# Optimization experiments

Measured on AMD Instinct MI355X. Metric: run time of the kernel, lower is better.

Reference implementation:

```python
import jax, jax.numpy as jnp
import numpy as np

N = 100000      # nodes
E = 1600000     # edges (avg degree 16)
IN = 128        # in_channels
OUT = 32        # out_channels -> hidden = 2*OUT = 64


def gcn_conv(x, src, dst, W, b):
    """PyG GCNConv: linear transform, add self loops, symmetric D^-1/2 (A+I) D^-1/2 aggregation."""
    n = x.shape[0]
    h = x @ W                                   # [N, out]
    # degree with self loops (all edge weights = 1)
    deg = jax.ops.segment_sum(jnp.ones(src.shape[0], h.dtype), dst, num_segments=n) + 1.0
    dinv = jax.lax.rsqrt(deg)                   # [N]
    norm = dinv[src] * dinv[dst]                # [E]
    agg = jax.ops.segment_sum(h[src] * norm[:, None], dst, num_segments=n)
    agg = agg + h * (dinv * dinv)[:, None]      # self-loop contribution
    return agg + b


def setup_inputs() -> dict:
    key = jax.random.key(0)
    ks = jax.random.split(key, 8)
    x = jax.random.normal(ks[0], (N, IN), jnp.float32)
    edge_index = jax.random.randint(ks[1], (2, E), 0, N, jnp.int32)
    H = 2 * OUT
    W1 = jax.random.normal(ks[2], (IN, H), jnp.float32) / jnp.sqrt(jnp.float32(IN))
    b1 = jnp.zeros((H,), jnp.float32)
    W_mu = jax.random.normal(ks[3], (H, OUT), jnp.float32) / jnp.sqrt(jnp.float32(H))
    b_mu = jnp.zeros((OUT,), jnp.float32)
    W_logstd = jax.random.normal(ks[4], (H, OUT), jnp.float32) / jnp.sqrt(jnp.float32(H))
    b_logstd = jnp.zeros((OUT,), jnp.float32)
    return {"x": x, "edge_index": edge_index, "W1": W1, "b1": b1,
            "W_mu": W_mu, "b_mu": b_mu, "W_logstd": W_logstd, "b_logstd": b_logstd}


def reference(x, edge_index, W1, b1, W_mu, b_mu, W_logstd, b_logstd):
    src, dst = edge_index[0], edge_index[1]
    h = jax.nn.relu(gcn_conv(x, src, dst, W1, b1))          # [N, 2*OUT]
    mu = gcn_conv(h, src, dst, W_mu, b_mu)                  # [N, OUT]
    logstd = gcn_conv(h, src, dst, W_logstd, b_logstd)      # [N, OUT]
    return mu, logstd
```

## Files before the change

### kernel.cpp

```cpp
#include <hip/hip_runtime.h>
#include <hip/hip_fp16.h>

#define IN_C 128
#define H 64
#define NBITS 9
#define BSZ 512
#define CAP 16384
#define BINCHUNK 4096

typedef unsigned int u32;
typedef __attribute__((ext_vector_type(8))) _Float16 h8;
typedef __attribute__((ext_vector_type(4))) float f4;

__device__ __forceinline__ int excl_scan256(int v, int* wsum, int tid) {
    int lane = tid & 63, wid = tid >> 6;
    int s = v;
    #pragma unroll
    for (int off = 1; off < 64; off <<= 1) {
        int t = __shfl_up(s, off);
        if (lane >= off) s += t;
    }
    if (lane == 63) wsum[wid] = s;
    __syncthreads();
    if (tid == 0) {
        int c = 0;
        #pragma unroll
        for (int i = 0; i < 4; ++i) { int t = wsum[i]; wsum[i] = c; c += t; }
    }
    __syncthreads();
    return s - v + wsum[wid];
}

__device__ __forceinline__ int excl_scan512(int v, int* wsum, int tid) {
    int lane = tid & 63, wid = tid >> 6;
    int s = v;
    #pragma unroll
    for (int off = 1; off < 64; off <<= 1) {
        int t = __shfl_up(s, off);
        if (lane >= off) s += t;
    }
    if (lane == 63) wsum[wid] = s;
    __syncthreads();
    if (tid == 0) {
        int c = 0;
        #pragma unroll
        for (int i = 0; i < 8; ++i) { int t = wsum[i]; wsum[i] = c; c += t; }
    }
    __syncthreads();
    return s - v + wsum[wid];
}

__global__ __launch_bounds__(256) void k_init(int* __restrict__ bucketFill,
                                              __half* __restrict__ z0,
                                              __half* __restrict__ z1,
                                              const float* __restrict__ W1,
                                              const float* __restrict__ Wmu,
                                              const float* __restrict__ Wls,
                                              _Float16* __restrict__ W1T,
                                              _Float16* __restrict__ WT2) {
    int tid = threadIdx.x;
    int gt = blockIdx.x * 256 + tid;
    if (blockIdx.x == 0) {
        bucketFill[tid] = 0;
        if (tid < H) { z0[tid] = __float2half(0.f); z1[tid] = __float2half(0.f); }
    }
    for (int t = gt; t < 64 * 128; t += gridDim.x * 256) {
        int col = t >> 7, k = t & 127;
        W1T[t] = (_Float16)W1[k * 64 + col];
    }
    for (int t = gt; t < 64 * 64; t += gridDim.x * 256) {
        int col = t >> 6, k = t & 63;
        WT2[t] = (_Float16)((col < 32) ? Wmu[k * 32 + col] : Wls[k * 32 + (col - 32)]);
    }
}

__device__ __forceinline__ void mm1_tile_mfma(int tile, int t256, int n,
                                              const float* __restrict__ x,
                                              const _Float16* __restrict__ W1T,
                                              __half* __restrict__ out) {
    int wave = t256 >> 6, lane = t256 & 63;
    int cl = lane & 15;
    int kg = lane >> 4;
    int arow = tile * 64 + wave * 16 + cl;
    int na = min(arow, n - 1);
    const float4* x4 = (const float4*)x;
    f4 zero4 = {0.f, 0.f, 0.f, 0.f};
    f4 acc[4] = {zero4, zero4, zero4, zero4};
    #pragma unroll
    for (int kb = 0; kb < 4; ++kb) {
        int k0 = kb * 32 + kg * 8;
        float4 va = x4[(size_t)na * 32 + (k0 >> 2)];
        float4 vb = x4[(size_t)na * 32 + (k0 >> 2) + 1];
        h8 a;
        a[0] = (_Float16)va.x; a[1] = (_Float16)va.y; a[2] = (_Float16)va.z; a[3] = (_Float16)va.w;
        a[4] = (_Float16)vb.x; a[5] = (_Float16)vb.y; a[6] = (_Float16)vb.z; a[7] = (_Float16)vb.w;
        #pragma unroll
        for (int c = 0; c < 4; ++c) {
            h8 b = *(const h8*)&W1T[((c * 16 + cl) << 7) + k0];
            acc[c] = __builtin_amdgcn_mfma_f32_16x16x32_f16(a, b, acc[c], 0, 0, 0);
        }
    }
    int rbase = tile * 64 + wave * 16 + kg * 4;
    #pragma unroll
    for (int r = 0; r < 4; ++r) {
        int orow = rbase + r;
        if (orow < n) {
            #pragma unroll
            for (int c = 0; c < 4; ++c)
                out[(size_t)orow * 64 + c * 16 + cl] = __float2half((float)acc[c][r]);
        }
    }
}

struct SMemBin {
    u32 staged[BINCHUNK]; unsigned char stagedB[BINCHUNK];
    int lhist[256], lbase[256], gbase[256], lfill[256]; int wsum[4];
};

__global__ __launch_bounds__(256) void k_binmm(const int* __restrict__ src,
                                               const int* __restrict__ dst,
                                               int E, int n, int nbin,
                                               int* __restrict__ bucketFill,
                                               u32* __restrict__ binned,
                                               const float* __restrict__ x,
                                               const _Float16* __restrict__ W1T,
                                               __half* __restrict__ Ah) {
    __shared__ SMemBin sm;
    int bid = blockIdx.x, tid = threadIdx.x;
    if (bid < nbin) {
        int kbeg = bid * BINCHUNK;
        int cnt = min(BINCHUNK, E - kbeg);
        sm.lhist[tid] = 0; sm.lfill[tid] = 0;
        __syncthreads();
        for (int t = tid; t < cnt; t += 256)
            atomicAdd(&sm.lhist[dst[kbeg + t] >> NBITS], 1);
        __syncthreads();
        int v = sm.lhist[tid];
        int ex = excl_scan256(v, sm.wsum, tid);
        sm.lbase[tid] = ex;
        sm.gbase[tid] = v ? atomicAdd(&bucketFill[tid], v) : 0;
        __syncthreads();
        for (int t = tid; t < cnt; t += 256) {
            int d = dst[kbeg + t];
            int s = src[kbeg + t];
            int bk = d >> NBITS;
            int p = sm.lbase[bk] + atomicAdd(&sm.lfill[bk], 1);
            sm.staged[p] = ((u32)(d & (BSZ - 1)) << 23) | (u32)s;
            sm.stagedB[p] = (unsigned char)bk;
        }
        __syncthreads();
        for (int t = tid; t < cnt; t += 256) {
            int bk = sm.stagedB[t];
            binned[(size_t)bk * CAP + sm.gbase[bk] + (t - sm.lbase[bk])] = sm.staged[t];
        }
    } else {
        mm1_tile_mfma(bid - nbin, tid, n, x, W1T, Ah);
    }
}

__global__ __launch_bounds__(512) void k_bucket(const u32* __restrict__ binned,
                                                const int* __restrict__ bucketFill,
                                                u32* __restrict__ rowdesc,
                                                float* __restrict__ dinvp,
                                                int* __restrict__ colidx,
                                                __half* __restrict__ Ah, int n) {
    __shared__ int cnt[BSZ];
    __shared__ int loff[BSZ];
    __shared__ float sdinv[BSZ];
    __shared__ int wsum[8];
    int b = blockIdx.x, tid = threadIdx.x;
    int ebeg = b * CAP;
    int fill = bucketFill[b];
    cnt[tid] = 0;
    __syncthreads();
    for (int e = tid; e < fill; e += 512)
        atomicAdd(&cnt[binned[ebeg + e] >> 23], 1);
    __syncthreads();
    int c0 = cnt[tid];
    int ex = excl_scan512(c0, wsum, tid);
    loff[tid] = ex;
    int node0 = (b << NBITS) + tid;
    float d0 = rsqrtf((float)c0 + 1.0f);
    sdinv[tid] = d0;
    if (node0 < n) {
        rowdesc[node0] = ((u32)(ebeg + ex) << 10) | (u32)min(c0, 1023);
        dinvp[node0] = d0;
    }
    __syncthreads();
    cnt[tid] = 0;
    __syncthreads();
    for (int e = tid; e < fill; e += 512) {
        u32 pv = binned[ebeg + e];
        int ln = pv >> 23;
        int pos = ebeg + loff[ln] + atomicAdd(&cnt[ln], 1);
        colidx[pos] = (int)(pv & 0x7FFFFF);
    }
    int nvalid = min(n - (b << NBITS), BSZ);
    uint2* rows = (uint2*)(Ah + ((size_t)b << NBITS) * 64);
    union U { uint2 u; __half2 h[2]; };
    for (int t = tid; t < nvalid * 16; t += 512) {
        float d = sdinv[t >> 4];
        U v; v.u = rows[t];
        float2 f0 = __half22float2(v.h[0]);
        float2 f1 = __half22float2(v.h[1]);
        v.h[0] = __floats2half2_rn(f0.x * d, f0.y * d);
        v.h[1] = __floats2half2_rn(f1.x * d, f1.y * d);
        rows[t] = v.u;
    }
}

template <bool L1, typename OutT>
__global__ __launch_bounds__(256) void k_gather(const __half* __restrict__ hs,
                                                OutT* __restrict__ out,
                                                const u32* __restrict__ rowdesc,
                                                const int* __restrict__ colidx,
                                                const float* __restrict__ dinv,
                                                const float* __restrict__ bias, int n) {
    int node = blockIdx.x * 4 + (threadIdx.x >> 6);
    if (node >= n) return;
    int lane = threadIdx.x & 63;
    int es = lane >> 4;
    int cc = lane & 15;
    u32 rd = rowdesc[node];
    int beg = (int)(rd >> 10);
    int deg = (int)(rd & 1023);
    int end = beg + deg;
    const uint2* hs4 = (const uint2*)hs;
    union U { uint2 u; __half2 h[2]; };

    int ci = n;
    if (lane < deg) ci = colidx[beg + lane];
    U selfr; selfr.u = hs4[(size_t)node * 16 + cc];
    float di = dinv[node];
    float a0 = 0.f, a1 = 0.f, a2 = 0.f, a3 = 0.f;

    {
        U r[8];
        #pragma unroll
        for (int j = 0; j < 8; ++j) {
            int s = __shfl(ci, 4 * j + es);
            r[j].u = hs4[(size_t)s * 16 + cc];
        }
        #pragma unroll
        for (int j = 0; j < 8; ++j) {
            float2 f0 = __half22float2(r[j].h[0]);
            float2 f1 = __half22float2(r[j].h[1]);
            a0 += f0.x; a1 += f0.y; a2 += f1.x; a3 += f1.y;
        }
    }
    if (deg > 32) {
        U r[8];
        #pragma unroll
        for (int j = 8; j < 16; ++j) {
            int s = __shfl(ci, (4 * j + es) & 63);
            r[j - 8].u = hs4[(size_t)s * 16 + cc];
        }
        #pragma unroll
        for (int j = 0; j < 8; ++j) {
            float2 f0 = __half22float2(r[j].h[0]);
            float2 f1 = __half22float2(r[j].h[1]);
            a0 += f0.x; a1 += f0.y; a2 += f1.x; a3 += f1.y;
        }
    }
    for (int e = beg + 64 + es; e < end; e += 4) {
        int s = colidx[e];
        U r; r.u = hs4[(size_t)s * 16 + cc];
        float2 f0 = __half22float2(r.h[0]);
        float2 f1 = __half22float2(r.h[1]);
        a0 += f0.x; a1 += f0.y; a2 += f1.x; a3 += f1.y;
    }
    a0 += __shfl_xor(a0, 16); a1 += __shfl_xor(a1, 16);
    a2 += __shfl_xor(a2, 16); a3 += __shfl_xor(a3, 16);
    a0 += __shfl_xor(a0, 32); a1 += __shfl_xor(a1, 32);
    a2 += __shfl_xor(a2, 32); a3 += __shfl_xor(a3, 32);

    if (lane < 16) {
        float2 f0 = __half22float2(selfr.h[0]);
        float2 f1 = __half22float2(selfr.h[1]);
        a0 += f0.x; a1 += f0.y; a2 += f1.x; a3 += f1.y;
        float v0 = di * a0, v1 = di * a1, v2 = di * a2, v3 = di * a3;
        if (L1) {
            float4 bv = ((const float4*)bias)[cc];
            v0 = fmaxf(v0 + bv.x, 0.f) * di;
            v1 = fmaxf(v1 + bv.y, 0.f) * di;
            v2 = fmaxf(v2 + bv.z, 0.f) * di;
            v3 = fmaxf(v3 + bv.w, 0.f) * di;
        }
        if constexpr (sizeof(OutT) == 2) {
            U o;
            o.h[0] = __floats2half2_rn(v0, v1);
            o.h[1] = __floats2half2_rn(v2, v3);
            ((uint2*)out)[(size_t)node * 16 + cc] = o.u;
        } else {
            ((float4*)out)[(size_t)node * 16 + cc] = make_float4(v0, v1, v2, v3);
        }
    }
}

__global__ __launch_bounds__(256) void k_mm2(const __half* __restrict__ G,
                                             const _Float16* __restrict__ WT2,
                                             const float* __restrict__ bmu,
                                             const float* __restrict__ bls,
                                             float* __restrict__ out, int n) {
    int tile = blockIdx.x;
    int wave = threadIdx.x >> 6, lane = threadIdx.x & 63;
    int cl = lane & 15, kg = lane >> 4;
    int arow = tile * 64 + wave * 16 + cl;
    int na = min(arow, n - 1);
    const _Float16* Gf = (const _Float16*)G;
    f4 zero4 = {0.f, 0.f, 0.f, 0.f};
    f4 acc[4] = {zero4, zero4, zero4, zero4};
    #pragma unroll
    for (int kb = 0; kb < 2; ++kb) {
        int k0 = kb * 32 + kg * 8;
        h8 a = *(const h8*)&Gf[((size_t)na << 6) + k0];
        #pragma unroll
        for (int c = 0; c < 4; ++c) {
            h8 b = *(const h8*)&WT2[((c * 16 + cl) << 6) + k0];
            acc[c] = __builtin_amdgcn_mfma_f32_16x16x32_f16(a, b, acc[c], 0, 0, 0);
        }
    }
    int rbase = tile * 64 + wave * 16 + kg * 4;
    #pragma unroll
    for (int c = 0; c < 4; ++c) {
        int col = c * 16 + cl;
        float bv = (col < 32) ? bmu[col] : bls[col - 32];
        float* obase = (col < 32) ? (out + col) : (out + (size_t)n * 32 + (col - 32));
        #pragma unroll
        for (int r = 0; r < 4; ++r) {
            int orow = rbase + r;
            if (orow < n) obase[(size_t)orow * 32] = (float)acc[c][r] + bv;
        }
    }
}


extern "C" void kernel_launch(void* const* d_in, const int* in_sizes, int n_in,
                              void* d_out, int out_size, void* d_ws, size_t ws_size,
                              hipStream_t stream) {
    const float* x   = (const float*)d_in[0];
    const int*   ei  = (const int*)d_in[1];
    const float* W1  = (const float*)d_in[2];
    const float* b1  = (const float*)d_in[3];
    const float* Wmu = (const float*)d_in[4];
    const float* bmu = (const float*)d_in[5];
    const float* Wls = (const float*)d_in[6];
    const float* bls = (const float*)d_in[7];
    float* out = (float*)d_out;

    int n = in_sizes[0] / IN_C;
    int E = in_sizes[1] / 2;
    const int* srcp = ei;
    const int* dstp = ei + E;
    int NBUK = (n + BSZ - 1) >> NBITS;
    int nbin = (E + BINCHUNK - 1) / BINCHUNK;
    int ntiles = (n + 63) / 64;

    char* p = (char*)d_ws;
    __half* Ah  = (__half*)p; p += (size_t)(n + 1) * H * sizeof(__half);
    __half* Bh  = (__half*)p; p += (size_t)(n + 1) * H * sizeof(__half);
    __half* G   = (__half*)p; p += (size_t)n * H * sizeof(__half);
    float* dinv = (float*)p;  p += (size_t)n * sizeof(float);
    u32* rowdesc = (u32*)p;   p += (size_t)n * sizeof(u32);
    int* colidx = (int*)p;    p += (size_t)NBUK * CAP * sizeof(int);
    u32* binned = (u32*)p;    p += (size_t)NBUK * CAP * sizeof(u32);
    int* bucketFill = (int*)p; p += 256 * sizeof(int);
    _Float16* W1T = (_Float16*)p; p += 64 * 128 * sizeof(_Float16);
    _Float16* WT2 = (_Float16*)p; p += 64 * 64 * sizeof(_Float16);

    k_init<<<16, 256, 0, stream>>>(bucketFill, Ah + (size_t)n * H, Bh + (size_t)n * H,
                                   W1, Wmu, Wls, W1T, WT2);
    k_binmm<<<nbin + ntiles, 256, 0, stream>>>(srcp, dstp, E, n, nbin,
                                               bucketFill, binned, x, W1T, Ah);
    k_bucket<<<NBUK, 512, 0, stream>>>(binned, bucketFill, rowdesc, dinv, colidx, Ah, n);

    k_gather<true, __half><<<(n + 3) / 4, 256, 0, stream>>>(Ah, Bh, rowdesc, colidx, dinv, b1, n);
    k_gather<false, __half><<<(n + 3) / 4, 256, 0, stream>>>(Bh, G, rowdesc, colidx, dinv, nullptr, n);
    k_mm2<<<(n + 63) / 64, 256, 0, stream>>>(G, WT2, bmu, bls, out, n);
}
```

Measured before the change: 243.8 us.

## Process four nodes per wave in gather with batched upfront loads

The gather kernel now assigns four consecutive nodes to each wavefront. It first loads all four row descriptors, dinv values, self rows and column indices, then issues the first 16 neighbor-row gathers for every node before any accumulation starts. The aim is more memory-level parallelism per wave and less per-node launch and latency overhead. The first unconditional batch shrinks from 32 to 16 neighbors, with an extra conditional batch for degree above 16. This raises register pressure and may reduce occupancy.

```diff
diff --git a/kernel.cpp b/kernel.cpp
--- a/kernel.cpp
+++ b/kernel.cpp
@@ -216,83 +216,112 @@
                                                 const int* __restrict__ colidx,
                                                 const float* __restrict__ dinv,
                                                 const float* __restrict__ bias, int n) {
-    int node = blockIdx.x * 4 + (threadIdx.x >> 6);
-    if (node >= n) return;
-    int lane = threadIdx.x & 63;
+    int wid = threadIdx.x >> 6, lane = threadIdx.x & 63;
+    int nbase = blockIdx.x * 16 + wid * 4;
+    if (nbase >= n) return;
     int es = lane >> 4;
     int cc = lane & 15;
-    u32 rd = rowdesc[node];
-    int beg = (int)(rd >> 10);
-    int deg = (int)(rd & 1023);
-    int end = beg + deg;
     const uint2* hs4 = (const uint2*)hs;
     union U { uint2 u; __half2 h[2]; };
 
-    int ci = n;
-    if (lane < deg) ci = colidx[beg + lane];
-    U selfr; selfr.u = hs4[(size_t)node * 16 + cc];
-    float di = dinv[node];
-    float a0 = 0.f, a1 = 0.f, a2 = 0.f, a3 = 0.f;
-
-    {
-        U r[8];
-        #pragma unroll
-        for (int j = 0; j < 8; ++j) {
-            int s = __shfl(ci, 4 * j + es);
-            r[j].u = hs4[(size_t)s * 16 + cc];
-        }
-        #pragma unroll
-        for (int j = 0; j < 8; ++j) {
-            float2 f0 = __half22float2(r[j].h[0]);
-            float2 f1 = __half22float2(r[j].h[1]);
+    u32 rdv[4]; float div_[4]; U selfv[4]; int civ[4];
+    #pragma unroll
+    for (int i = 0; i < 4; ++i) {
+        int node = min(nbase + i, n - 1);
+        rdv[i] = rowdesc[node];
+        div_[i] = dinv[node];
+        selfv[i].u = hs4[(size_t)node * 16 + cc];
+    }
+    #pragma unroll
+    for (int i = 0; i < 4; ++i) {
+        int beg = (int)(rdv[i] >> 10), deg = (int)(rdv[i] & 1023);
+        civ[i] = (lane < deg) ? colidx[beg + lane] : n;
+    }
+    U r0[4][4];
+    #pragma unroll
+    for (int i = 0; i < 4; ++i) {
+        #pragma unroll
+        for (int j = 0; j < 4; ++j) {
+            int s = __shfl(civ[i], 4 * j + es);
+            r0[i][j].u = hs4[(size_t)s * 16 + cc];
+        }
+    }
+
+    #pragma unroll
+    for (int i = 0; i < 4; ++i) {
+        int node = nbase + i;
+        if (node >= n) break;
+        int beg = (int)(rdv[i] >> 10);
+        int deg = (int)(rdv[i] & 1023);
+        int end = beg + deg;
+        float a0 = 0.f, a1 = 0.f, a2 = 0.f, a3 = 0.f;
+        #pragma unroll
+        for (int j = 0; j < 4; ++j) {
+            float2 f0 = __half22float2(r0[i][j].h[0]);
+            float2 f1 = __half22float2(r0[i][j].h[1]);
             a0 += f0.x; a1 += f0.y; a2 += f1.x; a3 += f1.y;
         }
-    }
-    if (deg > 32) {
-        U r[8];
-        #pragma unroll
-        for (int j = 8; j < 16; ++j) {
-            int s = __shfl(ci, (4 * j + es) & 63);
-            r[j - 8].u = hs4[(size_t)s * 16 + cc];
-        }
-        #pragma unroll
-        for (int j = 0; j < 8; ++j) {
-            float2 f0 = __half22float2(r[j].h[0]);
-            float2 f1 = __half22float2(r[j].h[1]);
+        if (deg > 16) {
+            U r[4];
+            #pragma unroll
+            for (int j = 4; j < 8; ++j) {
+                int s = __shfl(civ[i], 4 * j + es);
+                r[j - 4].u = hs4[(size_t)s * 16 + cc];
+            }
+            #pragma unroll
+            for (int j = 0; j < 4; ++j) {
+                float2 f0 = __half22float2(r[j].h[0]);
+                float2 f1 = __half22float2(r[j].h[1]);
+                a0 += f0.x; a1 += f0.y; a2 += f1.x; a3 += f1.y;
+            }
+        }
+        if (deg > 32) {
+            U r[8];
+            #pragma unroll
+            for (int j = 8; j < 16; ++j) {
+                int s = __shfl(civ[i], (4 * j + es) & 63);
+                r[j - 8].u = hs4[(size_t)s * 16 + cc];
+            }
+            #pragma unroll
+            for (int j = 0; j < 8; ++j) {
+                float2 f0 = __half22float2(r[j].h[0]);
+                float2 f1 = __half22float2(r[j].h[1]);
+                a0 += f0.x; a1 += f0.y; a2 += f1.x; a3 += f1.y;
+            }
+        }
+        for (int e = beg + 64 + es; e < end; e += 4) {
+            int s = colidx[e];
+            U r; r.u = hs4[(size_t)s * 16 + cc];
+            float2 f0 = __half22float2(r.h[0]);
+            float2 f1 = __half22float2(r.h[1]);
             a0 += f0.x; a1 += f0.y; a2 += f1.x; a3 += f1.y;
         }
-    }
-    for (int e = beg + 64 + es; e < end; e += 4) {
-        int s = colidx[e];
-        U r; r.u = hs4[(size_t)s * 16 + cc];
-        float2 f0 = __half22float2(r.h[0]);
-        float2 f1 = __half22float2(r.h[1]);
-        a0 += f0.x; a1 += f0.y; a2 += f1.x; a3 += f1.y;
-    }
-    a0 += __shfl_xor(a0, 16); a1 += __shfl_xor(a1, 16);
-    a2 += __shfl_xor(a2, 16); a3 += __shfl_xor(a3, 16);
-    a0 += __shfl_xor(a0, 32); a1 += __shfl_xor(a1, 32);
-    a2 += __shfl_xor(a2, 32); a3 += __shfl_xor(a3, 32);
-
-    if (lane < 16) {
-        float2 f0 = __half22float2(selfr.h[0]);
-        float2 f1 = __half22float2(selfr.h[1]);
-        a0 += f0.x; a1 += f0.y; a2 += f1.x; a3 += f1.y;
-        float v0 = di * a0, v1 = di * a1, v2 = di * a2, v3 = di * a3;
-        if (L1) {
-            float4 bv = ((const float4*)bias)[cc];
-            v0 = fmaxf(v0 + bv.x, 0.f) * di;
-            v1 = fmaxf(v1 + bv.y, 0.f) * di;
-            v2 = fmaxf(v2 + bv.z, 0.f) * di;
-            v3 = fmaxf(v3 + bv.w, 0.f) * di;
-        }
-        if constexpr (sizeof(OutT) == 2) {
-            U o;
-            o.h[0] = __floats2half2_rn(v0, v1);
-            o.h[1] = __floats2half2_rn(v2, v3);
-            ((uint2*)out)[(size_t)node * 16 + cc] = o.u;
-        } else {
-            ((float4*)out)[(size_t)node * 16 + cc] = make_float4(v0, v1, v2, v3);
+        a0 += __shfl_xor(a0, 16); a1 += __shfl_xor(a1, 16);
+        a2 += __shfl_xor(a2, 16); a3 += __shfl_xor(a3, 16);
+        a0 += __shfl_xor(a0, 32); a1 += __shfl_xor(a1, 32);
+        a2 += __shfl_xor(a2, 32); a3 += __shfl_xor(a3, 32);
+
+        if (lane < 16) {
+            float di = div_[i];
+            float2 f0 = __half22float2(selfv[i].h[0]);
+            float2 f1 = __half22float2(selfv[i].h[1]);
+            a0 += f0.x; a1 += f0.y; a2 += f1.x; a3 += f1.y;
+            float v0 = di * a0, v1 = di * a1, v2 = di * a2, v3 = di * a3;
+            if (L1) {
+                float4 bv = ((const float4*)bias)[cc];
+                v0 = fmaxf(v0 + bv.x, 0.f) * di;
+                v1 = fmaxf(v1 + bv.y, 0.f) * di;
+                v2 = fmaxf(v2 + bv.z, 0.f) * di;
+                v3 = fmaxf(v3 + bv.w, 0.f) * di;
+            }
+            if constexpr (sizeof(OutT) == 2) {
+                U o;
+                o.h[0] = __floats2half2_rn(v0, v1);
+                o.h[1] = __floats2half2_rn(v2, v3);
+                ((uint2*)out)[(size_t)node * 16 + cc] = o.u;
+            } else {
+                ((float4*)out)[(size_t)node * 16 + cc] = make_float4(v0, v1, v2, v3);
+            }
         }
     }
 }
@@ -374,7 +403,7 @@
                                                bucketFill, binned, x, W1T, Ah);
     k_bucket<<<NBUK, 512, 0, stream>>>(binned, bucketFill, rowdesc, dinv, colidx, Ah, n);
 
-    k_gather<true, __half><<<(n + 3) / 4, 256, 0, stream>>>(Ah, Bh, rowdesc, colidx, dinv, b1, n);
-    k_gather<false, __half><<<(n + 3) / 4, 256, 0, stream>>>(Bh, G, rowdesc, colidx, dinv, nullptr, n);
+    k_gather<true, __half><<<(n + 15) / 16, 256, 0, stream>>>(Ah, Bh, rowdesc, colidx, dinv, b1, n);
+    k_gather<false, __half><<<(n + 15) / 16, 256, 0, stream>>>(Bh, G, rowdesc, colidx, dinv, nullptr, n);
     k_mm2<<<(n + 63) / 64, 256, 0, stream>>>(G, WT2, bmu, bls, out, n);
 }
```

After: 244.1 us. About the same (+0.1%).
